# Kernel optimization log

Hardware: AMD Instinct MI355X
Metric: run time of the kernel (lower is better)

The kernel has to match this reference:

```python
import jax, jax.numpy as jnp
import numpy as np

N, M, D, G = 8192, 8192, 512, 10

def _embed_distance_matrix(dist):
    # classical MDS embedding: ||e_i - e_j||^2 == dist[i,j]**2
    g = dist.shape[0]
    d2 = dist ** 2
    J = np.eye(g) - np.ones((g, g)) / g
    B = -0.5 * J @ d2 @ J
    w, v = np.linalg.eigh(B)
    w = np.clip(w, 0.0, None)
    return (v * np.sqrt(w)).astype(np.float32)  # [g, g]

def setup_inputs() -> dict:
    key = jax.random.key(0)
    k1, k2, k3, k4 = jax.random.split(key, 4)
    X = jax.random.normal(k1, (N, D), dtype=jnp.float32)
    Z = jax.random.normal(k2, (M, D), dtype=jnp.float32)
    groupsX = jax.random.randint(k3, (N,), 0, G)
    groupsZ = jax.random.randint(k4, (M,), 0, G)
    group_distances = np.ones((G, G)) - np.eye(G)
    embedding = jnp.asarray(_embed_distance_matrix(group_distances))
    return {
        "X": X, "Z": Z,
        "groupsX": groupsX, "groupsZ": groupsZ,
        "embedding": embedding,
        "sigma": jnp.float32(1.0),
        "lengthscale": jnp.float32(1.0),
        "group_diff_param": jnp.float32(1.0),
    }

def _pairwise_sqdist(a, b):
    # ||a_i - b_j||^2 via GEMM; avoids the O(N*M*d) diff tensor
    aa = jnp.sum(a * a, axis=-1)  # [N]
    bb = jnp.sum(b * b, axis=-1)  # [M]
    return aa[:, None] + bb[None, :] - 2.0 * (a @ b.T)  # [N, M]

def reference(X, Z, groupsX, groupsZ, embedding, sigma, lengthscale, group_diff_param):
    p = X.shape[-1]
    ex = embedding[groupsX]  # [N, g]
    ez = embedding[groupsZ]  # [M, g]
    dist = _pairwise_sqdist(X, Z)           # [N, M]
    gdist = _pairwise_sqdist(ex, ez)        # [N, M]
    val = 1.0 / (jnp.abs(group_diff_param) * gdist + 1.0)
    dist_scaled = dist / lengthscale ** 2
    K = sigma ** 2 * jnp.exp(-0.5 * dist_scaled * val) * val ** (0.5 * p)
    return K  # [N, M], matches torch result.transpose(-1, 0)
```

## Files before the change

### kernel.cpp

```cpp
#include <hip/hip_runtime.h>
#include <hip/hip_bf16.h>
#include <cstdint>
#include <cstddef>

#define NROWS 8192
#define MCOLS 8192
#define DDIM  512
#define GRP   10

using f32x16 = __attribute__((ext_vector_type(16))) float;
using i32x4  = __attribute__((ext_vector_type(4))) int;
using i32x8  = __attribute__((ext_vector_type(8))) int;

typedef const __attribute__((address_space(1))) void* gas_ptr;
typedef __attribute__((address_space(3))) void* las_ptr;

__global__ __launch_bounds__(256) void prep_all(const float* __restrict__ X,
                                                const float* __restrict__ Z,
                                                uint16_t* __restrict__ Xa,
                                                uint16_t* __restrict__ Za,
                                                float* __restrict__ xx,
                                                float* __restrict__ zz,
                                                const float* __restrict__ emb,
                                                const float* __restrict__ sigma_p,
                                                const float* __restrict__ ls_p,
                                                const float* __restrict__ gdp_p,
                                                float2* __restrict__ tab) {
    int row = blockIdx.x;
    int t = threadIdx.x;
    if (row == 2 * NROWS) {
        if (t >= GRP * GRP) return;
        int a = t / GRP, b = t % GRP;
        float gd = 0.0f;
        #pragma unroll
        for (int g = 0; g < GRP; ++g) {
            float d = emb[a * GRP + g] - emb[b * GRP + g];
            gd += d * d;
        }
        float val = 1.0f / (fabsf(*gdp_p) * gd + 1.0f);
        float ls = *ls_p;
        float sg = *sigma_p;
        tab[t] = make_float2(-0.5f * val / (ls * ls),
                             sg * sg * powf(val, 0.5f * (float)DDIM));
        return;
    }
    const float* src;
    uint16_t* dst;
    float* sums;
    int r;
    if (row < NROWS) {
        r = row; src = X + (size_t)r * DDIM; dst = Xa + (size_t)r * (DDIM / 2); sums = xx;
    } else {
        r = row - NROWS; src = Z + (size_t)r * DDIM; dst = Za + (size_t)r * (DDIM / 2); sums = zz;
    }
    float2 p = ((const float2*)src)[t];
    int packed = __builtin_amdgcn_cvt_pk_fp8_f32(p.x, p.y, 0, false);
    dst[t] = (uint16_t)packed;
    float s = p.x * p.x + p.y * p.y;
    #pragma unroll
    for (int off = 32; off > 0; off >>= 1) s += __shfl_down(s, off, 64);
    __shared__ float ws[4];
    if ((t & 63) == 0) ws[t >> 6] = s;
    __syncthreads();
    if (t == 0) sums[r] = ws[0] + ws[1] + ws[2] + ws[3];
}

__global__ __launch_bounds__(256, 3) void mggp_gemm(
    const uint8_t* __restrict__ Xa, const uint8_t* __restrict__ Za,
    const float* __restrict__ xx, const float* __restrict__ zz,
    const int* __restrict__ gX, const int* __restrict__ gZ,
    const float2* __restrict__ tab,
    float* __restrict__ out) {

    __shared__ __align__(16) uint8_t Al[128 * 128];
    __shared__ __align__(16) uint8_t Bl[128 * 128];

    const int tid  = threadIdx.x;
    const int lane = tid & 63;
    const int w    = tid >> 6;
    const int wr   = w >> 1;
    const int wc   = w & 1;
    const int cl   = lane & 31;
    const int hi   = lane >> 5;

    const int lin = blockIdx.x;
    const int st  = lin >> 6;
    const int wi  = lin & 63;
    const int bx  = (st & 7) * 8 + (wi & 7);
    const int by  = (st >> 3) * 8 + (wi >> 3);
    const int brow = by * 128;
    const int bcol = bx * 128;

    f32x16 acc[2][2];
    #pragma unroll
    for (int ti = 0; ti < 2; ++ti)
        #pragma unroll
        for (int tj = 0; tj < 2; ++tj)
            #pragma unroll
            for (int e = 0; e < 16; ++e) acc[ti][tj][e] = 0.0f;

    for (int kt = 0; kt < DDIM / 128; ++kt) {
        __syncthreads();
        #pragma unroll
        for (int p = 0; p < 4; ++p) {
            int sbase = (w * 4 + p) * 64;
            int s = sbase + lane;
            int r = s >> 3;
            int c = (s & 7) ^ (r & 7);
            const uint8_t* ga = Xa + (size_t)(brow + r) * DDIM + kt * 128 + c * 16;
            __builtin_amdgcn_global_load_lds((gas_ptr)ga, (las_ptr)&Al[sbase * 16], 16, 0, 0);
            const uint8_t* gb = Za + (size_t)(bcol + r) * DDIM + kt * 128 + c * 16;
            __builtin_amdgcn_global_load_lds((gas_ptr)gb, (las_ptr)&Bl[sbase * 16], 16, 0, 0);
        }
        __syncthreads();

        #pragma unroll
        for (int kk = 0; kk < 2; ++kk) {
            i32x8 aF[2], bF[2];
            #pragma unroll
            for (int ti = 0; ti < 2; ++ti) {
                int r  = wr * 64 + ti * 32 + cl;
                int c1 = (kk * 4 + hi * 2) ^ (r & 7);
                i32x4 lo = *(const i32x4*)&Al[r * 128 + c1 * 16];
                i32x4 h4 = *(const i32x4*)&Al[r * 128 + (c1 ^ 1) * 16];
                aF[ti] = __builtin_shufflevector(lo, h4, 0, 1, 2, 3, 4, 5, 6, 7);
            }
            #pragma unroll
            for (int tj = 0; tj < 2; ++tj) {
                int r  = wc * 64 + tj * 32 + cl;
                int c1 = (kk * 4 + hi * 2) ^ (r & 7);
                i32x4 lo = *(const i32x4*)&Bl[r * 128 + c1 * 16];
                i32x4 h4 = *(const i32x4*)&Bl[r * 128 + (c1 ^ 1) * 16];
                bF[tj] = __builtin_shufflevector(lo, h4, 0, 1, 2, 3, 4, 5, 6, 7);
            }
            #pragma unroll
            for (int ti = 0; ti < 2; ++ti)
                #pragma unroll
                for (int tj = 0; tj < 2; ++tj)
                    acc[ti][tj] = __builtin_amdgcn_mfma_scale_f32_32x32x64_f8f6f4(
                        aF[ti], bF[tj], acc[ti][tj],
                        0, 0,
                        0, 0x7F7F7F7F,
                        0, 0x7F7F7F7F);
        }
    }

    float zzv[2];
    int   gbv[2];
    #pragma unroll
    for (int tj = 0; tj < 2; ++tj) {
        int j = bcol + wc * 64 + tj * 32 + cl;
        zzv[tj] = zz[j];
        gbv[tj] = gZ[j];
    }
    #pragma unroll
    for (int ti = 0; ti < 2; ++ti) {
        #pragma unroll
        for (int reg = 0; reg < 16; ++reg) {
            int i = brow + wr * 64 + ti * 32 + (reg & 3) + 8 * (reg >> 2) + 4 * hi;
            float xxi = xx[i];
            int   ga  = gX[i] * GRP;
            float* orow = out + (size_t)i * MCOLS + bcol + wc * 64 + cl;
            #pragma unroll
            for (int tj = 0; tj < 2; ++tj) {
                float dot  = acc[ti][tj][reg];
                float dist = xxi + zzv[tj] - 2.0f * dot;
                float2 tc  = tab[ga + gbv[tj]];
                orow[tj * 32] = tc.y * __expf(dist * tc.x);
            }
        }
    }
}

extern "C" void kernel_launch(void* const* d_in, const int* in_sizes, int n_in,
                              void* d_out, int out_size, void* d_ws, size_t ws_size,
                              hipStream_t stream) {
    const float* X     = (const float*)d_in[0];
    const float* Z     = (const float*)d_in[1];
    const int*   gX    = (const int*)d_in[2];
    const int*   gZ    = (const int*)d_in[3];
    const float* emb   = (const float*)d_in[4];
    const float* sigma = (const float*)d_in[5];
    const float* ls    = (const float*)d_in[6];
    const float* gdp   = (const float*)d_in[7];

    char* ws = (char*)d_ws;
    const size_t XA_OFF  = 0;
    const size_t ZA_OFF  = XA_OFF + (size_t)NROWS * DDIM;
    const size_t XX_OFF  = ZA_OFF + (size_t)MCOLS * DDIM;
    const size_t ZZ_OFF  = XX_OFF + (size_t)NROWS * 4;
    const size_t TAB_OFF = ZZ_OFF + (size_t)MCOLS * 4;

    uint8_t* Xa  = (uint8_t*)(ws + XA_OFF);
    uint8_t* Za  = (uint8_t*)(ws + ZA_OFF);
    float* xx    = (float*)(ws + XX_OFF);
    float* zz    = (float*)(ws + ZZ_OFF);
    float2* tab  = (float2*)(ws + TAB_OFF);

    prep_all<<<2 * NROWS + 1, 256, 0, stream>>>(X, Z, (uint16_t*)Xa, (uint16_t*)Za,
                                                xx, zz, emb, sigma, ls, gdp, tab);
    mggp_gemm<<<4096, 256, 0, stream>>>(Xa, Za, xx, zz, gX, gZ, tab, (float*)d_out);
}
```

Before: 340.7 us.

## Pre-pack FP8 operands into fragment-chunked layout and load MFMA fragments directly from global

The prep kernel now writes the FP8 copies of X and Z into a chunked layout in which each 32-byte K-slice of each row sits contiguously, grouped per MFMA K-step. The GEMM kernel drops its LDS staging, swizzling and barriers and has every lane load its A/B fragments straight from global memory, relying on L2/cache reuse across waves and blocks. This removes LDS traffic and synchronisation but duplicates global loads per wave, with no software prefetch, and the loads may be poorly coalesced (32-byte strided per lane).

```diff
diff --git a/kernel.cpp b/kernel.cpp
--- a/kernel.cpp
+++ b/kernel.cpp
@@ -8,12 +8,11 @@
 #define DDIM  512
 #define GRP   10
 
+#define CHUNK 262144
+
 using f32x16 = __attribute__((ext_vector_type(16))) float;
 using i32x4  = __attribute__((ext_vector_type(4))) int;
 using i32x8  = __attribute__((ext_vector_type(8))) int;
-
-typedef const __attribute__((address_space(1))) void* gas_ptr;
-typedef __attribute__((address_space(3))) void* las_ptr;
 
 __global__ __launch_bounds__(256) void prep_all(const float* __restrict__ X,
                                                 const float* __restrict__ Z,
@@ -49,13 +48,13 @@
     float* sums;
     int r;
     if (row < NROWS) {
-        r = row; src = X + (size_t)r * DDIM; dst = Xa + (size_t)r * (DDIM / 2); sums = xx;
+        r = row; src = X + (size_t)r * DDIM; dst = Xa; sums = xx;
     } else {
-        r = row - NROWS; src = Z + (size_t)r * DDIM; dst = Za + (size_t)r * (DDIM / 2); sums = zz;
+        r = row - NROWS; src = Z + (size_t)r * DDIM; dst = Za; sums = zz;
     }
     float2 p = ((const float2*)src)[t];
     int packed = __builtin_amdgcn_cvt_pk_fp8_f32(p.x, p.y, 0, false);
-    dst[t] = (uint16_t)packed;
+    dst[(size_t)(t >> 4) * (CHUNK / 2) + (size_t)r * 16 + (t & 15)] = (uint16_t)packed;
     float s = p.x * p.x + p.y * p.y;
     #pragma unroll
     for (int off = 32; off > 0; off >>= 1) s += __shfl_down(s, off, 64);
@@ -71,9 +70,6 @@
     const int* __restrict__ gX, const int* __restrict__ gZ,
     const float2* __restrict__ tab,
     float* __restrict__ out) {
-
-    __shared__ __align__(16) uint8_t Al[128 * 128];
-    __shared__ __align__(16) uint8_t Bl[128 * 128];
 
     const int tid  = threadIdx.x;
     const int lane = tid & 63;
@@ -99,50 +95,41 @@
             #pragma unroll
             for (int e = 0; e < 16; ++e) acc[ti][tj][e] = 0.0f;
 
-    for (int kt = 0; kt < DDIM / 128; ++kt) {
-        __syncthreads();
+    int va[2], vb[2];
+    #pragma unroll
+    for (int ti = 0; ti < 2; ++ti)
+        va[ti] = (brow + wr * 64 + ti * 32 + cl) * 32 + hi * CHUNK;
+    #pragma unroll
+    for (int tj = 0; tj < 2; ++tj)
+        vb[tj] = (bcol + wc * 64 + tj * 32 + cl) * 32 + hi * CHUNK;
+
+    #pragma unroll
+    for (int kt = 0; kt < 8; ++kt) {
+        const size_t ko = (size_t)kt * (2 * CHUNK);
+        i32x8 aF[2], bF[2];
         #pragma unroll
-        for (int p = 0; p < 4; ++p) {
-            int sbase = (w * 4 + p) * 64;
-            int s = sbase + lane;
-            int r = s >> 3;
-            int c = (s & 7) ^ (r & 7);
-            const uint8_t* ga = Xa + (size_t)(brow + r) * DDIM + kt * 128 + c * 16;
-            __builtin_amdgcn_global_load_lds((gas_ptr)ga, (las_ptr)&Al[sbase * 16], 16, 0, 0);
-            const uint8_t* gb = Za + (size_t)(bcol + r) * DDIM + kt * 128 + c * 16;
-            __builtin_amdgcn_global_load_lds((gas_ptr)gb, (las_ptr)&Bl[sbase * 16], 16, 0, 0);
+        for (int ti = 0; ti < 2; ++ti) {
+            const uint8_t* p = Xa + ko + va[ti];
+            i32x4 lo = *(const i32x4*)p;
+            i32x4 h4 = *(const i32x4*)(p + 16);
+            aF[ti] = __builtin_shufflevector(lo, h4, 0, 1, 2, 3, 4, 5, 6, 7);
         }
-        __syncthreads();
-
         #pragma unroll
-        for (int kk = 0; kk < 2; ++kk) {
-            i32x8 aF[2], bF[2];
+        for (int tj = 0; tj < 2; ++tj) {
+            const uint8_t* p = Za + ko + vb[tj];
+            i32x4 lo = *(const i32x4*)p;
+            i32x4 h4 = *(const i32x4*)(p + 16);
+            bF[tj] = __builtin_shufflevector(lo, h4, 0, 1, 2, 3, 4, 5, 6, 7);
+        }
+        #pragma unroll
+        for (int ti = 0; ti < 2; ++ti)
             #pragma unroll
-            for (int ti = 0; ti < 2; ++ti) {
-                int r  = wr * 64 + ti * 32 + cl;
-                int c1 = (kk * 4 + hi * 2) ^ (r & 7);
-                i32x4 lo = *(const i32x4*)&Al[r * 128 + c1 * 16];
-                i32x4 h4 = *(const i32x4*)&Al[r * 128 + (c1 ^ 1) * 16];
-                aF[ti] = __builtin_shufflevector(lo, h4, 0, 1, 2, 3, 4, 5, 6, 7);
-            }
-            #pragma unroll
-            for (int tj = 0; tj < 2; ++tj) {
-                int r  = wc * 64 + tj * 32 + cl;
-                int c1 = (kk * 4 + hi * 2) ^ (r & 7);
-                i32x4 lo = *(const i32x4*)&Bl[r * 128 + c1 * 16];
-                i32x4 h4 = *(const i32x4*)&Bl[r * 128 + (c1 ^ 1) * 16];
-                bF[tj] = __builtin_shufflevector(lo, h4, 0, 1, 2, 3, 4, 5, 6, 7);
-            }
-            #pragma unroll
-            for (int ti = 0; ti < 2; ++ti)
-                #pragma unroll
-                for (int tj = 0; tj < 2; ++tj)
-                    acc[ti][tj] = __builtin_amdgcn_mfma_scale_f32_32x32x64_f8f6f4(
-                        aF[ti], bF[tj], acc[ti][tj],
-                        0, 0,
-                        0, 0x7F7F7F7F,
-                        0, 0x7F7F7F7F);
-        }
+            for (int tj = 0; tj < 2; ++tj)
+                acc[ti][tj] = __builtin_amdgcn_mfma_scale_f32_32x32x64_f8f6f4(
+                    aF[ti], bF[tj], acc[ti][tj],
+                    0, 0,
+                    0, 0x7F7F7F7F,
+                    0, 0x7F7F7F7F);
     }
 
     float zzv[2];
```

Measured after the change: 347.1 us. About the same (+1.9%).
